# Performance work log

Measured on AMD Instinct MI355X. Metric: run time of the kernel, lower is better.

## Reference

```python
import jax, jax.numpy as jnp
import numpy as np

N_NODES = 50000
N_EDGES = 1600000
IN_CH = 512
OUT_CH = 48


def setup_inputs() -> dict:
    key = jax.random.key(0)
    k1, k2, k3, k4 = jax.random.split(key, 4)
    edge_index = jax.random.randint(k1, (2, N_EDGES), 0, N_NODES, dtype=jnp.int64)
    features = jax.random.normal(k2, (N_NODES, IN_CH), dtype=jnp.float32)
    edge_weights = jax.random.uniform(k3, (N_EDGES,), dtype=jnp.float32)
    # glorot-initialized weight, zero bias (as in reset_parameters)
    stdv = float(np.sqrt(6.0 / (IN_CH + OUT_CH)))
    weight = jax.random.uniform(k4, (IN_CH, OUT_CH), dtype=jnp.float32,
                                minval=-stdv, maxval=stdv)
    bias = jnp.zeros((OUT_CH,), dtype=jnp.float32)
    return {"edge_index": edge_index, "features": features,
            "edge_weights": edge_weights, "weight": weight, "bias": bias}


def reference(edge_index, features, edge_weights, weight, bias):
    # dense projection: [N, in] @ [in, out] -> [N, out]
    xw = jnp.matmul(features, weight)
    src, dst = edge_index[0], edge_index[1]
    # message: norm * x_j, gathered from source nodes  -> [E, out]
    msgs = edge_weights[:, None] * xw[src]
    # aggregate (add) at target nodes -> [N, out]
    aggr = jax.ops.segment_sum(msgs, dst, num_segments=N_NODES)
    z = aggr + bias
    return jax.nn.log_softmax(z, axis=1)
```

## Files before the change

### kernel.cpp

```cpp
#include <hip/hip_runtime.h>
#include <math.h>

#define N_NODES 50000
#define N_EDGES 1600000
#define IN_CH   512
#define OUT_CH  48
#define XW_LD   64
#define N_TILES (N_NODES / 16)

#define BSHIFT  6
#define BNODES  64
#define NB      ((N_NODES + BNODES - 1) / BNODES)
#define ETILE   4096
#define CAP     2816
#define CHUNK   128

#define BFRAG_SHORTS (16 * 3 * 64 * 8)
#define GEMM_BLOCKS ((N_TILES + 3) / 4)
#define HIST_BLOCKS 256

typedef __attribute__((ext_vector_type(8))) short bf16x8;
typedef __attribute__((ext_vector_type(4))) float f32x4;

static __device__ inline short f2bf(float x) {
    union { float f; unsigned u; } in; in.f = x;
    unsigned r = in.u + 0x7fffu + ((in.u >> 16) & 1u);
    return (short)(r >> 16);
}
static __device__ inline float bf2f(unsigned v16) {
    union { unsigned u; float f; } o; o.u = v16 << 16; return o.f;
}

__global__ __launch_bounds__(256) void prep_bfrag(const float* __restrict__ w,
                                                  unsigned short* __restrict__ wfrag) {
    int i = blockIdx.x * blockDim.x + threadIdx.x;
    if (i >= IN_CH * OUT_CH / 4) return;
    int flat = i * 4;
    int k   = flat / OUT_CH;
    int col = flat % OUT_CH;
    float4 v = *reinterpret_cast<const float4*>(w + flat);
    int s = k >> 5, j = k & 7, q = (k >> 3) & 3;
    float vv[4] = {v.x, v.y, v.z, v.w};
    #pragma unroll
    for (int c = 0; c < 4; ++c) {
        int cc = col + c;
        int t  = cc >> 4;
        int ln = (cc & 15) | (q << 4);
        wfrag[((s * 3 + t) * 64 + ln) * 8 + j] = (unsigned short)f2bf(vv[c]);
    }
}

static __device__ void gemm_body(char* smem, const float* __restrict__ f,
                                 const unsigned short* __restrict__ wfrag,
                                 unsigned short* __restrict__ xw) {
    short* sBl = reinterpret_cast<short*>(smem);

    int tid  = threadIdx.x;
    int lane = tid & 63;
    int wid  = tid >> 6;

    {
        const uint4* gw = reinterpret_cast<const uint4*>(wfrag);
        uint4*       sw = reinterpret_cast<uint4*>(smem);
        #pragma unroll
        for (int i = 0; i < BFRAG_SHORTS / 8 / 256; ++i)
            sw[i * 256 + tid] = gw[i * 256 + tid];
    }
    __syncthreads();

    int tile = blockIdx.x * 4 + wid;
    if (tile >= N_TILES) return;

    const bf16x8* sB = reinterpret_cast<const bf16x8*>(sBl);

    int row = tile * 16 + (lane & 15);
    const float* fp = f + (size_t)row * IN_CH + ((lane >> 4) << 3);

    f32x4 acc0 = {0.f, 0.f, 0.f, 0.f};
    f32x4 acc1 = {0.f, 0.f, 0.f, 0.f};
    f32x4 acc2 = {0.f, 0.f, 0.f, 0.f};

    float4 a0[2], a1[2];
    a0[0] = *reinterpret_cast<const float4*>(fp);
    a1[0] = *reinterpret_cast<const float4*>(fp + 4);

    #pragma unroll
    for (int s = 0; s < 16; ++s) {
        const int cb = s & 1, nb = cb ^ 1;
        if (s + 1 < 16) {
            a0[nb] = *reinterpret_cast<const float4*>(fp + (s + 1) * 32);
            a1[nb] = *reinterpret_cast<const float4*>(fp + (s + 1) * 32 + 4);
        }
        bf16x8 a;
        a[0] = f2bf(a0[cb].x); a[1] = f2bf(a0[cb].y);
        a[2] = f2bf(a0[cb].z); a[3] = f2bf(a0[cb].w);
        a[4] = f2bf(a1[cb].x); a[5] = f2bf(a1[cb].y);
        a[6] = f2bf(a1[cb].z); a[7] = f2bf(a1[cb].w);
        bf16x8 b0 = sB[(s * 3 + 0) * 64 + lane];
        bf16x8 b1 = sB[(s * 3 + 1) * 64 + lane];
        bf16x8 b2 = sB[(s * 3 + 2) * 64 + lane];
        acc0 = __builtin_amdgcn_mfma_f32_16x16x32_bf16(a, b0, acc0, 0, 0, 0);
        acc1 = __builtin_amdgcn_mfma_f32_16x16x32_bf16(a, b1, acc1, 0, 0, 0);
        acc2 = __builtin_amdgcn_mfma_f32_16x16x32_bf16(a, b2, acc2, 0, 0, 0);
    }

    unsigned short* orow = xw + (size_t)tile * 16 * XW_LD;
    int c  = lane & 15;
    int r0 = (lane >> 4) * 4;
    #pragma unroll
    for (int r = 0; r < 4; ++r) {
        orow[(size_t)(r0 + r) * XW_LD +  0 + c] = (unsigned short)f2bf(acc0[r]);
        orow[(size_t)(r0 + r) * XW_LD + 16 + c] = (unsigned short)f2bf(acc1[r]);
        orow[(size_t)(r0 + r) * XW_LD + 32 + c] = (unsigned short)f2bf(acc2[r]);
    }
}

static __device__ void hist_body(char* smem, int bid, const int* __restrict__ dst,
                                 int* __restrict__ counts) {
    int* hc = reinterpret_cast<int*>(smem);
    for (int i = threadIdx.x; i < NB; i += 256) hc[i] = 0;
    __syncthreads();
    for (int e = bid * 256 + threadIdx.x; e < N_EDGES; e += HIST_BLOCKS * 256)
        atomicAdd(&hc[dst[e] >> BSHIFT], 1);
    __syncthreads();
    for (int i = threadIdx.x; i < NB; i += 256)
        if (hc[i]) atomicAdd(&counts[i], hc[i]);
}

__global__ __launch_bounds__(256) void gemm_hist(const float* __restrict__ f,
                                                 const unsigned short* __restrict__ wfrag,
                                                 unsigned short* __restrict__ xw,
                                                 const int* __restrict__ dst,
                                                 int* __restrict__ counts) {
    __shared__ __align__(16) char smem[BFRAG_SHORTS * 2];
    if (blockIdx.x < GEMM_BLOCKS) gemm_body(smem, f, wfrag, xw);
    else                          hist_body(smem, blockIdx.x - GEMM_BLOCKS, dst, counts);
}

__global__ __launch_bounds__(1024) void bucket_scan(const int* __restrict__ counts,
                                                    int* __restrict__ base,
                                                    int* __restrict__ cursor) {
    __shared__ int sdata[1024];
    int t = threadIdx.x;
    int i0 = 2 * t, i1 = 2 * t + 1;
    int v0 = (i0 < NB) ? counts[i0] : 0;
    int v1 = (i1 < NB) ? counts[i1] : 0;
    int s = v0 + v1;
    sdata[t] = s;
    __syncthreads();
    for (int d = 1; d < 1024; d <<= 1) {
        int x = (t >= d) ? sdata[t - d] : 0;
        __syncthreads();
        sdata[t] += x;
        __syncthreads();
    }
    int excl = sdata[t] - s;
    if (i0 < NB) { base[i0] = excl;      cursor[i0] = excl; }
    if (i1 < NB) { base[i1] = excl + v0; cursor[i1] = excl + v0; }
}

__global__ __launch_bounds__(512) void bin_edges(const int* __restrict__ src,
                                                 const int* __restrict__ dst,
                                                 const float* __restrict__ ew,
                                                 int* __restrict__ cursor,
                                                 int2* __restrict__ epack) {
    __shared__ int   hist[NB];
    __shared__ int   loff[NB];
    __shared__ int   gbase[NB];
    __shared__ int   ssum[512];
    __shared__ int2  buf[ETILE];
    __shared__ short bkt[ETILE];

    int tid = threadIdx.x;
    int tileStart = blockIdx.x * ETILE;
    int tileN = N_EDGES - tileStart; if (tileN > ETILE) tileN = ETILE;

    for (int i = tid; i < NB; i += 512) hist[i] = 0;
    __syncthreads();

    int rank[ETILE / 512];
    int dreg[ETILE / 512];
    #pragma unroll
    for (int k = 0; k < ETILE / 512; ++k) {
        int e = tileStart + k * 512 + tid;
        dreg[k] = (e < N_EDGES) ? dst[e] : 0;
        rank[k] = (e < N_EDGES) ? atomicAdd(&hist[dreg[k] >> BSHIFT], 1) : 0;
    }
    __syncthreads();

    for (int i = tid; i < NB; i += 512) {
        int c = hist[i];
        gbase[i] = c ? atomicAdd(&cursor[i], c) : 0;
    }

    int a0 = (2 * tid     < NB) ? hist[2 * tid]     : 0;
    int a1 = (2 * tid + 1 < NB) ? hist[2 * tid + 1] : 0;
    ssum[tid] = a0 + a1;
    __syncthreads();
    for (int d = 1; d < 512; d <<= 1) {
        int x = (tid >= d) ? ssum[tid - d] : 0;
        __syncthreads();
        ssum[tid] += x;
        __syncthreads();
    }
    int excl = ssum[tid] - (a0 + a1);
    if (2 * tid     < NB) loff[2 * tid]     = excl;
    if (2 * tid + 1 < NB) loff[2 * tid + 1] = excl + a0;
    __syncthreads();

    #pragma unroll
    for (int k = 0; k < ETILE / 512; ++k) {
        int e = tileStart + k * 512 + tid;
        if (e < N_EDGES) {
            int d = dreg[k];
            int b = d >> BSHIFT;
            int slot = loff[b] + rank[k];
            int2 p;
            p.x = (src[e] & 0xFFFF) | (d << 16);
            p.y = __float_as_int(ew[e]);
            buf[slot] = p;
            bkt[slot] = (short)b;
        }
    }
    __syncthreads();

    for (int idx = tid; idx < tileN; idx += 512) {
        int b = bkt[idx];
        epack[gbase[b] + idx - loff[b]] = buf[idx];
    }
}

__global__ __launch_bounds__(512) void sort_bucket(const int* __restrict__ base,
                                                   const int* __restrict__ cursor,
                                                   int2* __restrict__ epack) {
    __shared__ int2  A[CAP];
    __shared__ int2  B[CAP];
    __shared__ short rk[CAP];
    __shared__ int   hist[BNODES];
    __shared__ int   loff[BNODES];

    int b  = blockIdx.x;
    int lo = base[b], hi = cursor[b];
    int len = hi - lo;
    if (len <= 0 || len > CAP) return;

    int tid = threadIdx.x;
    if (tid < BNODES) hist[tid] = 0;
    for (int i = tid; i < len; i += 512) A[i] = epack[lo + i];
    __syncthreads();

    for (int i = tid; i < len; i += 512) {
        int key = (((unsigned)A[i].x) >> 16) & (BNODES - 1);
        rk[i] = (short)atomicAdd(&hist[key], 1);
    }
    __syncthreads();

    if (tid < BNODES) {
        int v = hist[tid];
        int s = v;
        #pragma unroll
        for (int d = 1; d < 64; d <<= 1) {
            int t = __shfl_up(s, d);
            if (tid >= d) s += t;
        }
        loff[tid] = s - v;
    }
    __syncthreads();

    for (int i = tid; i < len; i += 512) {
        int key = (((unsigned)A[i].x) >> 16) & (BNODES - 1);
        B[loff[key] + rk[i]] = A[i];
    }
    __syncthreads();

    for (int i = tid; i < len; i += 512) epack[lo + i] = B[i];
}

__global__ __launch_bounds__(512) void seg_aggregate(const int2* __restrict__ epack,
                                                     const unsigned short* __restrict__ xw,
                                                     float* __restrict__ out) {
    int wv   = (blockIdx.x * blockDim.x + threadIdx.x) >> 6;
    int lane = threadIdx.x & 63;
    int base = wv * CHUNK;
    if (base >= N_EDGES) return;
    int h  = lane >> 5;
    int cp = lane & 31;
    bool act = (cp < 24);

    int2 E0 = epack[base + lane];
    int2 E1 = epack[base + 64 + lane];

    float ax = 0.f, ay = 0.f;
    int cur = ((unsigned)__shfl(E0.x, h)) >> 16;

    int px[2][8]; float pw[2][8]; unsigned u[2][8];

    #pragma unroll
    for (int k = 0; k < 8; ++k) {
        int idx = ((2 * k) & 63) | h;
        px[0][k] = __shfl(E0.x, idx);
        pw[0][k] = __int_as_float(__shfl(E0.y, idx));
    }
    #pragma unroll
    for (int k = 0; k < 8; ++k)
        u[0][k] = *reinterpret_cast<const unsigned*>(
            xw + (size_t)(px[0][k] & 0xFFFF) * XW_LD + (cp << 1));

    #pragma unroll
    for (int j = 0; j < 8; ++j) {
        const int cb = j & 1, nb = cb ^ 1;
        if (j + 1 < 8) {
            #pragma unroll
            for (int k = 0; k < 8; ++k) {
                int t  = (j + 1) * 8 + k;
                int sx = (t < 32) ? E0.x : E1.x;
                int sy = (t < 32) ? E0.y : E1.y;
                int idx = ((2 * t) & 63) | h;
                px[nb][k] = __shfl(sx, idx);
                pw[nb][k] = __int_as_float(__shfl(sy, idx));
            }
            #pragma unroll
            for (int k = 0; k < 8; ++k)
                u[nb][k] = *reinterpret_cast<const unsigned*>(
                    xw + (size_t)(px[nb][k] & 0xFFFF) * XW_LD + (cp << 1));
        }
        #pragma unroll
        for (int k = 0; k < 8; ++k) {
            int node = ((unsigned)px[cb][k]) >> 16;
            if (node != cur) {
                if (act) {
                    atomicAdd(&out[(size_t)cur * OUT_CH + (cp << 1)    ], ax);
                    atomicAdd(&out[(size_t)cur * OUT_CH + (cp << 1) + 1], ay);
                }
                ax = 0.f; ay = 0.f; cur = node;
            }
            float    wf = pw[cb][k];
            unsigned uu = u[cb][k];
            ax = fmaf(wf, bf2f(uu & 0xFFFFu), ax);
            ay = fmaf(wf, bf2f(uu >> 16), ay);
        }
    }

    if (act) {
        atomicAdd(&out[(size_t)cur * OUT_CH + (cp << 1)    ], ax);
        atomicAdd(&out[(size_t)cur * OUT_CH + (cp << 1) + 1], ay);
    }
}

__global__ __launch_bounds__(256) void lsm_rows(float* __restrict__ z,
                                                const float* __restrict__ bias) {
    int node = (blockIdx.x * blockDim.x + threadIdx.x) >> 6;
    int lane = threadIdx.x & 63;
    if (node >= N_NODES) return;
    bool ch = (lane < OUT_CH);

    float v = ch ? (z[(size_t)node * OUT_CH + lane] + bias[lane]) : -INFINITY;
    float m = v;
    #pragma unroll
    for (int d = 32; d >= 1; d >>= 1) m = fmaxf(m, __shfl_xor(m, d));
    float e = ch ? expf(v - m) : 0.f;
    float s = e;
    #pragma unroll
    for (int d = 32; d >= 1; d >>= 1) s += __shfl_xor(s, d);
    float lse = m + logf(s);
    if (ch) z[(size_t)node * OUT_CH + lane] = v - lse;
}

extern "C" void kernel_launch(void* const* d_in, const int* in_sizes, int n_in,
                              void* d_out, int out_size, void* d_ws, size_t ws_size,
                              hipStream_t stream) {
    const int*   edge_index = (const int*)d_in[0];
    const float* features   = (const float*)d_in[1];
    const float* eweights   = (const float*)d_in[2];
    const float* weight     = (const float*)d_in[3];
    const float* bias       = (const float*)d_in[4];

    const int* src = edge_index;
    const int* dst = edge_index + N_EDGES;

    float* out = (float*)d_out;

    char* ws = (char*)d_ws;
    unsigned short* xw    = (unsigned short*)(ws + 0);
    int*   counts = (int*)  (ws + 9600000);
    int*   base   = (int*)  (ws + 9616000);
    int*   cursor = (int*)  (ws + 9632000);
    int2*  epack  = (int2*) (ws + 9648000);
    unsigned short* wfrag = (unsigned short*)(ws + 22448000);

    hipMemsetAsync(counts, 0, NB * sizeof(int), stream);
    hipMemsetAsync(d_out, 0, (size_t)N_NODES * OUT_CH * sizeof(float), stream);

    prep_bfrag<<<(IN_CH * OUT_CH / 4 + 255) / 256, 256, 0, stream>>>(weight, wfrag);

    gemm_hist<<<GEMM_BLOCKS + HIST_BLOCKS, 256, 0, stream>>>(features, wfrag, xw,
                                                             dst, counts);

    bucket_scan<<<1, 1024, 0, stream>>>(counts, base, cursor);
    bin_edges<<<(N_EDGES + ETILE - 1) / ETILE, 512, 0, stream>>>(src, dst, eweights,
                                                                 cursor, epack);
    sort_bucket<<<NB, 512, 0, stream>>>(base, cursor, epack);

    {
        int nWaves  = N_EDGES / CHUNK;
        int nBlocks = (nWaves + 7) / 8;
        seg_aggregate<<<nBlocks, 512, 0, stream>>>(epack, xw, out);
    }
    lsm_rows<<<(N_NODES + 3) / 4, 256, 0, stream>>>(out, bias);
}
```

Measured before the change: 145.9 us.

## Regroup kernels: fuse weight prep with histogram, GEMM with edge binning; halve aggregate chunk

Weight-fragment preparation now runs in the same launch as the destination histogram, and the feature GEMM now runs in the same launch as edge binning. The GEMM uses 512-thread blocks and shares one shared-memory buffer with the binning code. This removes one launch and lets the heavy GEMM overlap the bandwidth-bound binning instead of the small histogram. Separately, the segment-aggregate chunk is halved to 64 edges per wave, which doubles the wave count and the boundary atomics. The fused kernel's larger shared-memory footprint may lower occupancy for the GEMM blocks.

After: 144.2 us. Within noise of the previous version (-1.1%).

```diff
diff --git a/kernel.cpp b/kernel.cpp
--- a/kernel.cpp
+++ b/kernel.cpp
@@ -13,11 +13,14 @@
 #define NB      ((N_NODES + BNODES - 1) / BNODES)
 #define ETILE   4096
 #define CAP     2816
-#define CHUNK   128
+#define CHUNK   64
 
 #define BFRAG_SHORTS (16 * 3 * 64 * 8)
-#define GEMM_BLOCKS ((N_TILES + 3) / 4)
+
+#define PREP_BLOCKS 24
 #define HIST_BLOCKS 256
+#define GEMMB_BLOCKS ((N_TILES + 7) / 8)
+#define BIN_BLOCKS   ((N_EDGES + ETILE - 1) / ETILE)
 
 typedef __attribute__((ext_vector_type(8))) short bf16x8;
 typedef __attribute__((ext_vector_type(4))) float f32x4;
@@ -31,9 +34,9 @@
     union { unsigned u; float f; } o; o.u = v16 << 16; return o.f;
 }
 
-__global__ __launch_bounds__(256) void prep_bfrag(const float* __restrict__ w,
-                                                  unsigned short* __restrict__ wfrag) {
-    int i = blockIdx.x * blockDim.x + threadIdx.x;
+static __device__ void prep_body(const float* __restrict__ w,
+                                 unsigned short* __restrict__ wfrag) {
+    int i = blockIdx.x * 256 + threadIdx.x;
     if (i >= IN_CH * OUT_CH / 4) return;
     int flat = i * 4;
     int k   = flat / OUT_CH;
@@ -50,9 +53,47 @@
     }
 }
 
-static __device__ void gemm_body(char* smem, const float* __restrict__ f,
-                                 const unsigned short* __restrict__ wfrag,
-                                 unsigned short* __restrict__ xw) {
+__global__ __launch_bounds__(256) void prep_hist(const float* __restrict__ w,
+                                                 unsigned short* __restrict__ wfrag,
+                                                 const int* __restrict__ dst,
+                                                 int* __restrict__ counts) {
+    __shared__ int hc[NB];
+    if (blockIdx.x < PREP_BLOCKS) { prep_body(w, wfrag); return; }
+    int bid = blockIdx.x - PREP_BLOCKS;
+    for (int i = threadIdx.x; i < NB; i += 256) hc[i] = 0;
+    __syncthreads();
+    for (int e = bid * 256 + threadIdx.x; e < N_EDGES; e += HIST_BLOCKS * 256)
+        atomicAdd(&hc[dst[e] >> BSHIFT], 1);
+    __syncthreads();
+    for (int i = threadIdx.x; i < NB; i += 256)
+        if (hc[i]) atomicAdd(&counts[i], hc[i]);
+}
+
+__global__ __launch_bounds__(1024) void bucket_scan(const int* __restrict__ counts,
+                                                    int* __restrict__ base,
+                                                    int* __restrict__ cursor) {
+    __shared__ int sdata[1024];
+    int t = threadIdx.x;
+    int i0 = 2 * t, i1 = 2 * t + 1;
+    int v0 = (i0 < NB) ? counts[i0] : 0;
+    int v1 = (i1 < NB) ? counts[i1] : 0;
+    int s = v0 + v1;
+    sdata[t] = s;
+    __syncthreads();
+    for (int d = 1; d < 1024; d <<= 1) {
+        int x = (t >= d) ? sdata[t - d] : 0;
+        __syncthreads();
+        sdata[t] += x;
+        __syncthreads();
+    }
+    int excl = sdata[t] - s;
+    if (i0 < NB) { base[i0] = excl;      cursor[i0] = excl; }
+    if (i1 < NB) { base[i1] = excl + v0; cursor[i1] = excl + v0; }
+}
+
+static __device__ void gemm_body512(char* smem, const float* __restrict__ f,
+                                    const unsigned short* __restrict__ wfrag,
+                                    unsigned short* __restrict__ xw) {
     short* sBl = reinterpret_cast<short*>(smem);
 
     int tid  = threadIdx.x;
@@ -63,12 +104,12 @@
         const uint4* gw = reinterpret_cast<const uint4*>(wfrag);
         uint4*       sw = reinterpret_cast<uint4*>(smem);
         #pragma unroll
-        for (int i = 0; i < BFRAG_SHORTS / 8 / 256; ++i)
-            sw[i * 256 + tid] = gw[i * 256 + tid];
-    }
-    __syncthreads();
-
-    int tile = blockIdx.x * 4 + wid;
+        for (int i = 0; i < BFRAG_SHORTS / 8 / 512; ++i)
+            sw[i * 512 + tid] = gw[i * 512 + tid];
+    }
+    __syncthreads();
+
+    int tile = blockIdx.x * 8 + wid;
     if (tile >= N_TILES) return;
 
     const bf16x8* sB = reinterpret_cast<const bf16x8*>(sBl);
@@ -115,64 +156,18 @@
     }
 }
 
-static __device__ void hist_body(char* smem, int bid, const int* __restrict__ dst,
-                                 int* __restrict__ counts) {
-    int* hc = reinterpret_cast<int*>(smem);
-    for (int i = threadIdx.x; i < NB; i += 256) hc[i] = 0;
-    __syncthreads();
-    for (int e = bid * 256 + threadIdx.x; e < N_EDGES; e += HIST_BLOCKS * 256)
-        atomicAdd(&hc[dst[e] >> BSHIFT], 1);
-    __syncthreads();
-    for (int i = threadIdx.x; i < NB; i += 256)
-        if (hc[i]) atomicAdd(&counts[i], hc[i]);
-}
-
-__global__ __launch_bounds__(256) void gemm_hist(const float* __restrict__ f,
-                                                 const unsigned short* __restrict__ wfrag,
-                                                 unsigned short* __restrict__ xw,
-                                                 const int* __restrict__ dst,
-                                                 int* __restrict__ counts) {
-    __shared__ __align__(16) char smem[BFRAG_SHORTS * 2];
-    if (blockIdx.x < GEMM_BLOCKS) gemm_body(smem, f, wfrag, xw);
-    else                          hist_body(smem, blockIdx.x - GEMM_BLOCKS, dst, counts);
-}
-
-__global__ __launch_bounds__(1024) void bucket_scan(const int* __restrict__ counts,
-                                                    int* __restrict__ base,
-                                                    int* __restrict__ cursor) {
-    __shared__ int sdata[1024];
-    int t = threadIdx.x;
-    int i0 = 2 * t, i1 = 2 * t + 1;
-    int v0 = (i0 < NB) ? counts[i0] : 0;
-    int v1 = (i1 < NB) ? counts[i1] : 0;
-    int s = v0 + v1;
-    sdata[t] = s;
-    __syncthreads();
-    for (int d = 1; d < 1024; d <<= 1) {
-        int x = (t >= d) ? sdata[t - d] : 0;
-        __syncthreads();
-        sdata[t] += x;
-        __syncthreads();
-    }
-    int excl = sdata[t] - s;
-    if (i0 < NB) { base[i0] = excl;      cursor[i0] = excl; }
-    if (i1 < NB) { base[i1] = excl + v0; cursor[i1] = excl + v0; }
-}
-
-__global__ __launch_bounds__(512) void bin_edges(const int* __restrict__ src,
-                                                 const int* __restrict__ dst,
-                                                 const float* __restrict__ ew,
-                                                 int* __restrict__ cursor,
-                                                 int2* __restrict__ epack) {
-    __shared__ int   hist[NB];
-    __shared__ int   loff[NB];
-    __shared__ int   gbase[NB];
-    __shared__ int   ssum[512];
-    __shared__ int2  buf[ETILE];
-    __shared__ short bkt[ETILE];
+static __device__ void bin_body(char* smem, int bid, const int* __restrict__ src,
+                                const int* __restrict__ dst, const float* __restrict__ ew,
+                                int* __restrict__ cursor, int2* __restrict__ epack) {
+    int*   hist  = reinterpret_cast<int*>(smem);
+    int*   loff  = reinterpret_cast<int*>(smem + 3200);
+    int*   gbase = reinterpret_cast<int*>(smem + 6400);
+    int*   ssum  = reinterpret_cast<int*>(smem + 9600);
+    int2*  buf   = reinterpret_cast<int2*>(smem + 11648);
+    short* bkt   = reinterpret_cast<short*>(smem + 44416);
 
     int tid = threadIdx.x;
-    int tileStart = blockIdx.x * ETILE;
+    int tileStart = bid * ETILE;
     int tileN = N_EDGES - tileStart; if (tileN > ETILE) tileN = ETILE;
 
     for (int i = tid; i < NB; i += 512) hist[i] = 0;
@@ -230,6 +225,19 @@
     }
 }
 
+__global__ __launch_bounds__(512) void gemm_bin(const float* __restrict__ f,
+                                                const unsigned short* __restrict__ wfrag,
+                                                unsigned short* __restrict__ xw,
+                                                const int* __restrict__ src,
+                                                const int* __restrict__ dst,
+                                                const float* __restrict__ ew,
+                                                int* __restrict__ cursor,
+                                                int2* __restrict__ epack) {
+    __shared__ __align__(16) char smem[52608];
+    if (blockIdx.x < GEMMB_BLOCKS) gemm_body512(smem, f, wfrag, xw);
+    else bin_body(smem, blockIdx.x - GEMMB_BLOCKS, src, dst, ew, cursor, epack);
+}
+
 __global__ __launch_bounds__(512) void sort_bucket(const int* __restrict__ base,
                                                    const int* __restrict__ cursor,
                                                    int2* __restrict__ epack) {
@@ -288,7 +296,6 @@
     bool act = (cp < 24);
 
     int2 E0 = epack[base + lane];
-    int2 E1 = epack[base + 64 + lane];
 
     float ax = 0.f, ay = 0.f;
     int cur = ((unsigned)__shfl(E0.x, h)) >> 16;
@@ -297,7 +304,7 @@
 
     #pragma unroll
     for (int k = 0; k < 8; ++k) {
-        int idx = ((2 * k) & 63) | h;
+        int idx = (2 * k) | h;
         px[0][k] = __shfl(E0.x, idx);
         pw[0][k] = __int_as_float(__shfl(E0.y, idx));
     }
@@ -307,17 +314,15 @@
             xw + (size_t)(px[0][k] & 0xFFFF) * XW_LD + (cp << 1));
 
     #pragma unroll
-    for (int j = 0; j < 8; ++j) {
+    for (int j = 0; j < 4; ++j) {
         const int cb = j & 1, nb = cb ^ 1;
-        if (j + 1 < 8) {
+        if (j + 1 < 4) {
             #pragma unroll
             for (int k = 0; k < 8; ++k) {
                 int t  = (j + 1) * 8 + k;
-                int sx = (t < 32) ? E0.x : E1.x;
-                int sy = (t < 32) ? E0.y : E1.y;
-                int idx = ((2 * t) & 63) | h;
-                px[nb][k] = __shfl(sx, idx);
-                pw[nb][k] = __int_as_float(__shfl(sy, idx));
+                int idx = (2 * t) | h;
+                px[nb][k] = __shfl(E0.x, idx);
+                pw[nb][k] = __int_as_float(__shfl(E0.y, idx));
             }
             #pragma unroll
             for (int k = 0; k < 8; ++k)
@@ -391,14 +396,13 @@
     hipMemsetAsync(counts, 0, NB * sizeof(int), stream);
     hipMemsetAsync(d_out, 0, (size_t)N_NODES * OUT_CH * sizeof(float), stream);
 
-    prep_bfrag<<<(IN_CH * OUT_CH / 4 + 255) / 256, 256, 0, stream>>>(weight, wfrag);
-
-    gemm_hist<<<GEMM_BLOCKS + HIST_BLOCKS, 256, 0, stream>>>(features, wfrag, xw,
-                                                             dst, counts);
+    prep_hist<<<PREP_BLOCKS + HIST_BLOCKS, 256, 0, stream>>>(weight, wfrag, dst, counts);
 
     bucket_scan<<<1, 1024, 0, stream>>>(counts, base, cursor);
-    bin_edges<<<(N_EDGES + ETILE - 1) / ETILE, 512, 0, stream>>>(src, dst, eweights,
-                                                                 cursor, epack);
+    gemm_bin<<<GEMMB_BLOCKS + BIN_BLOCKS, 512, 0, stream>>>(features, wfrag, xw,
+                                                            src, dst, eweights,
+                                                            cursor, epack);
+
     sort_bucket<<<NB, 512, 0, stream>>>(base, cursor, epack);
 
     {
```
